# Performance work log

Hardware: AMD Instinct MI355X
Metric: run time of the kernel (lower is better)

Reference implementation:

```python
import jax, jax.numpy as jnp
import numpy as np

N_NODES = 200000
N_EDGES = 3200000
N_FEAT = 602
N_CLASS = 41


def setup_inputs() -> dict:
    key = jax.random.key(0)
    k1, k2, k3 = jax.random.split(key, 3)
    x = jax.random.normal(k1, (N_NODES, N_FEAT), dtype=jnp.float32)
    W = jax.random.normal(k2, (N_FEAT, N_CLASS), dtype=jnp.float32) * (1.0 / np.sqrt(N_FEAT))
    b = jnp.zeros((N_CLASS,), dtype=jnp.float32)
    edge_index = jax.random.randint(k3, (2, N_EDGES), 0, N_NODES, dtype=jnp.int64)
    return {"x": x, "W": W, "b": b, "edge_index": edge_index}


def reference(x, W, b, edge_index):
    # GCNConv: add self-loops, symmetric normalization, linear transform,
    # scatter-add aggregation, bias; then log_softmax (module forward).
    N = x.shape[0]
    loops = jnp.arange(N, dtype=edge_index.dtype)
    src = jnp.concatenate([edge_index[0], loops])  # [E+N]
    dst = jnp.concatenate([edge_index[1], loops])  # [E+N]
    # degree of A + I computed on destination index
    deg = jax.ops.segment_sum(jnp.ones(src.shape, dtype=x.dtype), dst, num_segments=N)
    dinv = jax.lax.rsqrt(jnp.maximum(deg, 1.0))  # deg >= 1 due to self-loops
    norm = dinv[src] * dinv[dst]                 # [E+N]
    h = x @ W                                    # [N, C] transform before aggregation (C < F)
    msg = h[src] * norm[:, None]                 # [E+N, C]
    agg = jax.ops.segment_sum(msg, dst, num_segments=N) + b  # [N, C]
    z = jax.nn.log_softmax(agg, axis=1)
    return (agg, z)
```

## Files before the change

kernel.cpp:

```cpp
#include <hip/hip_runtime.h>
#include <hip/hip_bf16.h>
#include <math.h>

#define F 602
#define C 41
#define HP_STRIDE 64
#define KSTEPS 19
#define GROWS 64
#define ASTRIDE 616

typedef short short8 __attribute__((ext_vector_type(8)));
typedef float f32x4 __attribute__((ext_vector_type(4)));

static __device__ __forceinline__ unsigned short f2bf(float f){
  unsigned int x = __float_as_uint(f);
  x += 0x7FFFu + ((x >> 16) & 1u);
  return (unsigned short)(x >> 16);
}
static __device__ __forceinline__ float bf2f(unsigned short u){
  return __uint_as_float(((unsigned int)u) << 16);
}

__global__ void k_flag(const int* __restrict__ e32, int* __restrict__ flag){
  __shared__ int s[256];
  int t = threadIdx.x;
  int v = 0;
  for (int i = t; i < 2048; i += 256) v |= e32[2*i + 1];
  s[t] = v; __syncthreads();
  for (int off = 128; off > 0; off >>= 1){
    if (t < off) s[t] |= s[t + off];
    __syncthreads();
  }
  if (t == 0) flag[0] = (s[0] == 0) ? 1 : 0;
}

static __device__ __forceinline__ int eidx(const int* __restrict__ p, int is64, long long pos){
  return is64 ? p[2*pos] : p[pos];
}

__global__ void k_count(const int* __restrict__ ei, const int* __restrict__ flag,
                        int* __restrict__ count, int* __restrict__ epos, int E){
  int e = blockIdx.x * 256 + threadIdx.x;
  if (e >= E) return;
  int is64 = flag[0];
  int d = eidx(ei, is64, (long long)E + e);
  epos[e] = atomicAdd(&count[d], 1);
}

__global__ void k_scan1(const int* __restrict__ count, int* __restrict__ rs,
                        float* __restrict__ dinv, int* __restrict__ bsum, int N){
  __shared__ int s[256];
  int t = threadIdx.x;
  int base = blockIdx.x * 2048 + t * 8;
  int v[8]; int tot = 0;
  #pragma unroll
  for (int j = 0; j < 8; j++){
    int i = base + j;
    int c = (i < N) ? count[i] : 0;
    v[j] = c; tot += c;
    if (i < N) dinv[i] = rsqrtf((float)(c + 1));
  }
  s[t] = tot; __syncthreads();
  for (int off = 1; off < 256; off <<= 1){
    int x = (t >= off) ? s[t - off] : 0;
    __syncthreads();
    s[t] += x;
    __syncthreads();
  }
  int run = s[t] - tot;
  #pragma unroll
  for (int j = 0; j < 8; j++){
    int i = base + j;
    if (i < N) rs[i] = run;
    run += v[j];
  }
  if (t == 255) bsum[blockIdx.x] = s[255];
}

__global__ void k_scan2(int* __restrict__ bsum, int nb){
  __shared__ int s[256];
  int t = threadIdx.x;
  int v = (t < nb) ? bsum[t] : 0;
  s[t] = v; __syncthreads();
  for (int off = 1; off < 256; off <<= 1){
    int x = (t >= off) ? s[t - off] : 0;
    __syncthreads();
    s[t] += x;
    __syncthreads();
  }
  if (t < nb) bsum[t] = s[t] - v;
}

__global__ void k_scan3(int* __restrict__ rs, const int* __restrict__ bsum, int N, int E){
  int i = blockIdx.x * 256 + threadIdx.x;
  if (i == 0) rs[N] = E;
  if (i >= N) return;
  rs[i] = rs[i] + bsum[i >> 11];
}

__global__ void k_fill(const int* __restrict__ ei, const int* __restrict__ flag,
                       const int* __restrict__ epos, const int* __restrict__ rs,
                       int* __restrict__ csr, int E){
  int e = blockIdx.x * 256 + threadIdx.x;
  if (e >= E) return;
  int is64 = flag[0];
  int s = eidx(ei, is64, e);
  int d = eidx(ei, is64, (long long)E + e);
  csr[rs[d] + epos[e]] = s;
}

__global__ void k_wprep(const float* __restrict__ W, unsigned short* __restrict__ Wf){
  int idx = blockIdx.x * 256 + threadIdx.x;
  if (idx >= KSTEPS * 3 * 64) return;
  int lane = idx & 63;
  int nt = (idx >> 6) % 3;
  int s = idx / (3 * 64);
  int quad = lane >> 4, l16 = lane & 15;
  int n = nt * 16 + l16;
  unsigned int w[4];
  #pragma unroll
  for (int p = 0; p < 4; p++){
    int k0 = s * 32 + quad * 8 + 2 * p;
    float lo = (k0     < F && n < C) ? W[k0 * C + n]       : 0.f;
    float hi = (k0 + 1 < F && n < C) ? W[(k0 + 1) * C + n] : 0.f;
    w[p] = (unsigned)f2bf(lo) | ((unsigned)f2bf(hi) << 16);
  }
  ((uint4*)Wf)[idx] = make_uint4(w[0], w[1], w[2], w[3]);
}

__global__ __launch_bounds__(256) void k_gemm3(const float* __restrict__ x,
        const unsigned short* __restrict__ Wf, unsigned short* __restrict__ hp, int N){
  __shared__ unsigned short As[GROWS * ASTRIDE];
  const int t = threadIdx.x;
  const long long rb0 = (long long)blockIdx.x * GROWS;
  for (int i = t; i < GROWS * 6; i += 256){
    int r = i / 6, c = 602 + (i - r * 6);
    As[r * ASTRIDE + c] = 0;
  }
  long long nrow = (long long)N - rb0; if (nrow > GROWS) nrow = GROWS;
  const int limit = (int)(nrow * F);
  const float* base = x + rb0 * F;
  #pragma unroll 8
  for (int f4 = t; f4 * 4 < limit; f4 += 256){
    int idx = f4 * 4;
    f32x4 v = __builtin_nontemporal_load((const f32x4*)(base + idx));
    int row = idx / F;
    int col = idx - row * F;
    if (col <= F - 4){
      int a = row * ASTRIDE + col;
      unsigned p0 = (unsigned)f2bf(v[0]) | ((unsigned)f2bf(v[1]) << 16);
      unsigned p1 = (unsigned)f2bf(v[2]) | ((unsigned)f2bf(v[3]) << 16);
      *(unsigned*)&As[a]     = p0;
      *(unsigned*)&As[a + 2] = p1;
    } else {
      float e[4] = {v[0], v[1], v[2], v[3]};
      #pragma unroll
      for (int q = 0; q < 4; q++){
        int ii = idx + q;
        int r2 = ii / F, c2 = ii - r2 * F;
        As[r2 * ASTRIDE + c2] = f2bf(e[q]);
      }
    }
  }
  __syncthreads();
  const int wv = t >> 6, lane = t & 63;
  const int quad = lane >> 4, l16 = lane & 15;
  const unsigned short* arow = &As[(wv * 16 + l16) * ASTRIDE + quad * 8];
  const short8* wf8 = (const short8*)Wf;
  f32x4 acc0 = {0.f,0.f,0.f,0.f}, acc1 = acc0, acc2 = acc0;
  #pragma unroll
  for (int s = 0; s < KSTEPS; s++){
    short8 a  = *(const short8*)(arow + s * 32);
    short8 b0 = wf8[(s * 3 + 0) * 64 + lane];
    short8 b1 = wf8[(s * 3 + 1) * 64 + lane];
    short8 b2 = wf8[(s * 3 + 2) * 64 + lane];
    acc0 = __builtin_amdgcn_mfma_f32_16x16x32_bf16(a, b0, acc0, 0, 0, 0);
    acc1 = __builtin_amdgcn_mfma_f32_16x16x32_bf16(a, b1, acc1, 0, 0, 0);
    acc2 = __builtin_amdgcn_mfma_f32_16x16x32_bf16(a, b2, acc2, 0, 0, 0);
  }
  int rl = wv * 16 + quad * 4;
  #pragma unroll
  for (int reg = 0; reg < 4; reg++){
    long long grow = rb0 + rl + reg;
    if (grow < N){
      unsigned short* hr = hp + grow * HP_STRIDE;
      hr[0 * 16 + l16] = f2bf(acc0[reg]);
      hr[1 * 16 + l16] = f2bf(acc1[reg]);
      hr[2 * 16 + l16] = f2bf(acc2[reg]);
    }
  }
}

__global__ __launch_bounds__(256) void k_agg(const unsigned short* __restrict__ hp,
        const int* __restrict__ csr, const int* __restrict__ rs,
        const float* __restrict__ dinv, const float* __restrict__ b,
        float* __restrict__ agg, float* __restrict__ z, int N){
  int node = blockIdx.x * 4 + (threadIdx.x >> 6);
  int lane = threadIdx.x & 63;
  if (node >= N) return;
  int beg = rs[node], end = rs[node + 1];
  float dn = dinv[node];
  bool act = lane < C;
  const unsigned short* hb = hp + lane;
  float acc = 0.f;
  if (act) acc = dn * dn * bf2f(hb[(long long)node << 6]);
  int i = beg;
  for (; i + 7 < end; i += 8){
    int s0 = csr[i],   s1 = csr[i+1], s2 = csr[i+2], s3 = csr[i+3];
    int s4 = csr[i+4], s5 = csr[i+5], s6 = csr[i+6], s7 = csr[i+7];
    float n0 = dinv[s0] * dn, n1 = dinv[s1] * dn;
    float n2 = dinv[s2] * dn, n3 = dinv[s3] * dn;
    float n4 = dinv[s4] * dn, n5 = dinv[s5] * dn;
    float n6 = dinv[s6] * dn, n7 = dinv[s7] * dn;
    float h0 = 0.f, h1 = 0.f, h2 = 0.f, h3 = 0.f;
    float h4 = 0.f, h5 = 0.f, h6 = 0.f, h7 = 0.f;
    if (act){
      h0 = bf2f(hb[(long long)s0 << 6]);
      h1 = bf2f(hb[(long long)s1 << 6]);
      h2 = bf2f(hb[(long long)s2 << 6]);
      h3 = bf2f(hb[(long long)s3 << 6]);
      h4 = bf2f(hb[(long long)s4 << 6]);
      h5 = bf2f(hb[(long long)s5 << 6]);
      h6 = bf2f(hb[(long long)s6 << 6]);
      h7 = bf2f(hb[(long long)s7 << 6]);
    }
    acc = fmaf(n0, h0, acc); acc = fmaf(n1, h1, acc);
    acc = fmaf(n2, h2, acc); acc = fmaf(n3, h3, acc);
    acc = fmaf(n4, h4, acc); acc = fmaf(n5, h5, acc);
    acc = fmaf(n6, h6, acc); acc = fmaf(n7, h7, acc);
  }
  for (; i + 3 < end; i += 4){
    int s0 = csr[i], s1 = csr[i+1], s2 = csr[i+2], s3 = csr[i+3];
    float n0 = dinv[s0] * dn, n1 = dinv[s1] * dn;
    float n2 = dinv[s2] * dn, n3 = dinv[s3] * dn;
    float h0 = 0.f, h1 = 0.f, h2 = 0.f, h3 = 0.f;
    if (act){
      h0 = bf2f(hb[(long long)s0 << 6]);
      h1 = bf2f(hb[(long long)s1 << 6]);
      h2 = bf2f(hb[(long long)s2 << 6]);
      h3 = bf2f(hb[(long long)s3 << 6]);
    }
    acc = fmaf(n0, h0, acc); acc = fmaf(n1, h1, acc);
    acc = fmaf(n2, h2, acc); acc = fmaf(n3, h3, acc);
  }
  for (; i < end; i++){
    int s0 = csr[i];
    float n0 = dinv[s0] * dn;
    if (act) acc = fmaf(n0, bf2f(hb[(long long)s0 << 6]), acc);
  }
  float a = -3.0e38f;
  if (act){
    a = acc + b[lane];
    agg[(long long)node * C + lane] = a;
  }
  float m = a;
  #pragma unroll
  for (int off = 32; off > 0; off >>= 1) m = fmaxf(m, __shfl_xor(m, off, 64));
  float ex = act ? expf(a - m) : 0.f;
  float s = ex;
  #pragma unroll
  for (int off = 32; off > 0; off >>= 1) s += __shfl_xor(s, off, 64);
  if (act) z[(long long)node * C + lane] = a - m - logf(s);
}

extern "C" void kernel_launch(void* const* d_in, const int* in_sizes, int n_in,
                              void* d_out, int out_size, void* d_ws, size_t ws_size,
                              hipStream_t stream){
  const float* x = (const float*)d_in[0];
  const float* W = (const float*)d_in[1];
  const float* b = (const float*)d_in[2];
  const int*   ei = (const int*)d_in[3];
  int N = in_sizes[0] / F;
  int E = in_sizes[3] / 2;

  float* out = (float*)d_out;
  float* agg = out;
  float* z   = out + (long long)N * C;

  char* ws = (char*)d_ws;
  auto al = [](size_t v){ return (v + 255) & ~size_t(255); };
  size_t o = 0;
  int*   flag  = (int*)(ws + o);  o = al(o + 4);
  int*   count = (int*)(ws + o);  o = al(o + (size_t)N * 4);
  float* dinv  = (float*)(ws + o); o = al(o + (size_t)N * 4);
  int*   rs    = (int*)(ws + o);  o = al(o + ((size_t)N + 1) * 4);
  int*   bsum  = (int*)(ws + o);  o = al(o + 4096);
  unsigned short* Wf = (unsigned short*)(ws + o); o = al(o + (size_t)KSTEPS * 3 * 64 * 16);
  int*   epos  = (int*)(ws + o);  o = al(o + (size_t)E * 4);
  int*   csr   = (int*)(ws + o);  o = al(o + (size_t)E * 4);
  unsigned short* hp = (unsigned short*)(ws + o); o = al(o + (size_t)N * HP_STRIDE * 2);

  int nb_e    = (E + 255) / 256;
  int nb_scan = (N + 2047) / 2048;
  int nb_n    = (N + 255) / 256;
  int nb_g    = (N + GROWS - 1) / GROWS;
  int nb_node = (N + 3) / 4;
  int nb_w    = (KSTEPS * 3 * 64 + 255) / 256;

  k_flag<<<1, 256, 0, stream>>>(ei, flag);
  hipMemsetAsync(count, 0, (size_t)N * 4, stream);
  k_count<<<nb_e, 256, 0, stream>>>(ei, flag, count, epos, E);
  k_wprep<<<nb_w, 256, 0, stream>>>(W, Wf);
  k_scan1<<<nb_scan, 256, 0, stream>>>(count, rs, dinv, bsum, N);
  k_scan2<<<1, 256, 0, stream>>>(bsum, nb_scan);
  k_scan3<<<nb_n, 256, 0, stream>>>(rs, bsum, N, E);
  k_fill<<<nb_e, 256, 0, stream>>>(ei, flag, epos, rs, csr, E);
  k_gemm3<<<nb_g, 256, 0, stream>>>(x, Wf, hp, N);
  k_agg<<<nb_node, 256, 0, stream>>>(hp, csr, rs, dinv, b, agg, z, N);
}
```

Before: 1.083 ms.

## Fuse edge counting into GEMM kernel with 8-way split counters and merged scans

Folds the atomic edge-count pass into the GEMM launch, interleaving one GEMM block with every four count blocks so atomic latency overlaps the bandwidth-bound x read. Per-destination counters are split into 8 replicas keyed by edge index to cut atomic contention, and the scan reconstructs per-replica offsets for the fill. The GEMM now reads x directly from global memory into registers instead of staging it through LDS, and scan2 is merged into scan3. In exchange it uses more workspace and memset traffic for the 8x counters, and the direct loads are narrower and less coalesced.

```diff
diff --git a/kernel.cpp b/kernel.cpp
--- a/kernel.cpp
+++ b/kernel.cpp
@@ -7,10 +7,10 @@
 #define HP_STRIDE 64
 #define KSTEPS 19
 #define GROWS 64
-#define ASTRIDE 616
 
 typedef short short8 __attribute__((ext_vector_type(8)));
 typedef float f32x4 __attribute__((ext_vector_type(4)));
+typedef float f32x2 __attribute__((ext_vector_type(2)));
 
 static __device__ __forceinline__ unsigned short f2bf(float f){
   unsigned int x = __float_as_uint(f);
@@ -36,77 +36,6 @@
 
 static __device__ __forceinline__ int eidx(const int* __restrict__ p, int is64, long long pos){
   return is64 ? p[2*pos] : p[pos];
-}
-
-__global__ void k_count(const int* __restrict__ ei, const int* __restrict__ flag,
-                        int* __restrict__ count, int* __restrict__ epos, int E){
-  int e = blockIdx.x * 256 + threadIdx.x;
-  if (e >= E) return;
-  int is64 = flag[0];
-  int d = eidx(ei, is64, (long long)E + e);
-  epos[e] = atomicAdd(&count[d], 1);
-}
-
-__global__ void k_scan1(const int* __restrict__ count, int* __restrict__ rs,
-                        float* __restrict__ dinv, int* __restrict__ bsum, int N){
-  __shared__ int s[256];
-  int t = threadIdx.x;
-  int base = blockIdx.x * 2048 + t * 8;
-  int v[8]; int tot = 0;
-  #pragma unroll
-  for (int j = 0; j < 8; j++){
-    int i = base + j;
-    int c = (i < N) ? count[i] : 0;
-    v[j] = c; tot += c;
-    if (i < N) dinv[i] = rsqrtf((float)(c + 1));
-  }
-  s[t] = tot; __syncthreads();
-  for (int off = 1; off < 256; off <<= 1){
-    int x = (t >= off) ? s[t - off] : 0;
-    __syncthreads();
-    s[t] += x;
-    __syncthreads();
-  }
-  int run = s[t] - tot;
-  #pragma unroll
-  for (int j = 0; j < 8; j++){
-    int i = base + j;
-    if (i < N) rs[i] = run;
-    run += v[j];
-  }
-  if (t == 255) bsum[blockIdx.x] = s[255];
-}
-
-__global__ void k_scan2(int* __restrict__ bsum, int nb){
-  __shared__ int s[256];
-  int t = threadIdx.x;
-  int v = (t < nb) ? bsum[t] : 0;
-  s[t] = v; __syncthreads();
-  for (int off = 1; off < 256; off <<= 1){
-    int x = (t >= off) ? s[t - off] : 0;
-    __syncthreads();
-    s[t] += x;
-    __syncthreads();
-  }
-  if (t < nb) bsum[t] = s[t] - v;
-}
-
-__global__ void k_scan3(int* __restrict__ rs, const int* __restrict__ bsum, int N, int E){
-  int i = blockIdx.x * 256 + threadIdx.x;
-  if (i == 0) rs[N] = E;
-  if (i >= N) return;
-  rs[i] = rs[i] + bsum[i >> 11];
-}
-
-__global__ void k_fill(const int* __restrict__ ei, const int* __restrict__ flag,
-                       const int* __restrict__ epos, const int* __restrict__ rs,
-                       int* __restrict__ csr, int E){
-  int e = blockIdx.x * 256 + threadIdx.x;
-  if (e >= E) return;
-  int is64 = flag[0];
-  int s = eidx(ei, is64, e);
-  int d = eidx(ei, is64, (long long)E + e);
-  csr[rs[d] + epos[e]] = s;
 }
 
 __global__ void k_wprep(const float* __restrict__ W, unsigned short* __restrict__ Wf){
@@ -128,49 +57,55 @@
   ((uint4*)Wf)[idx] = make_uint4(w[0], w[1], w[2], w[3]);
 }
 
-__global__ __launch_bounds__(256) void k_gemm3(const float* __restrict__ x,
-        const unsigned short* __restrict__ Wf, unsigned short* __restrict__ hp, int N){
-  __shared__ unsigned short As[GROWS * ASTRIDE];
+__global__ __launch_bounds__(256) void k_front(const float* __restrict__ x,
+        const unsigned short* __restrict__ Wf, unsigned short* __restrict__ hp,
+        const int* __restrict__ ei, const int* __restrict__ flag,
+        int* __restrict__ cnt8, int* __restrict__ epos,
+        int N, int E, int nb_e, int nb_g){
+  const int bid = blockIdx.x;
+  const int g = bid / 5, r5 = bid - g * 5;
+  if (r5 < 4){
+    int cb = g * 4 + r5;
+    int e = cb * 256 + threadIdx.x;
+    if (cb >= nb_e || e >= E) return;
+    int is64 = flag[0];
+    int d = eidx(ei, is64, (long long)E + e);
+    int rr = e & 7;
+    epos[e] = atomicAdd(&cnt8[(size_t)rr * N + d], 1);
+    return;
+  }
+  if (g >= nb_g) return;
   const int t = threadIdx.x;
-  const long long rb0 = (long long)blockIdx.x * GROWS;
-  for (int i = t; i < GROWS * 6; i += 256){
-    int r = i / 6, c = 602 + (i - r * 6);
-    As[r * ASTRIDE + c] = 0;
-  }
-  long long nrow = (long long)N - rb0; if (nrow > GROWS) nrow = GROWS;
-  const int limit = (int)(nrow * F);
-  const float* base = x + rb0 * F;
-  #pragma unroll 8
-  for (int f4 = t; f4 * 4 < limit; f4 += 256){
-    int idx = f4 * 4;
-    f32x4 v = __builtin_nontemporal_load((const f32x4*)(base + idx));
-    int row = idx / F;
-    int col = idx - row * F;
-    if (col <= F - 4){
-      int a = row * ASTRIDE + col;
-      unsigned p0 = (unsigned)f2bf(v[0]) | ((unsigned)f2bf(v[1]) << 16);
-      unsigned p1 = (unsigned)f2bf(v[2]) | ((unsigned)f2bf(v[3]) << 16);
-      *(unsigned*)&As[a]     = p0;
-      *(unsigned*)&As[a + 2] = p1;
-    } else {
-      float e[4] = {v[0], v[1], v[2], v[3]};
-      #pragma unroll
-      for (int q = 0; q < 4; q++){
-        int ii = idx + q;
-        int r2 = ii / F, c2 = ii - r2 * F;
-        As[r2 * ASTRIDE + c2] = f2bf(e[q]);
-      }
-    }
-  }
-  __syncthreads();
   const int wv = t >> 6, lane = t & 63;
   const int quad = lane >> 4, l16 = lane & 15;
-  const unsigned short* arow = &As[(wv * 16 + l16) * ASTRIDE + quad * 8];
+  const long long rb0 = (long long)g * GROWS;
+  long long rowb = rb0 + wv * 16 + l16;
+  long long row = (rowb < N) ? rowb : (long long)(N - 1);
+  const float* xr = x + row * (long long)F;
   const short8* wf8 = (const short8*)Wf;
+  const int kq = quad * 8;
   f32x4 acc0 = {0.f,0.f,0.f,0.f}, acc1 = acc0, acc2 = acc0;
   #pragma unroll
   for (int s = 0; s < KSTEPS; s++){
-    short8 a  = *(const short8*)(arow + s * 32);
+    float xv0, xv1, xv2, xv3, xv4, xv5, xv6, xv7;
+    if (s < KSTEPS - 1 || quad < 3){
+      int k0 = s * 32 + kq;
+      f32x2 p0 = __builtin_nontemporal_load((const f32x2*)(xr + k0 + 0));
+      f32x2 p1 = __builtin_nontemporal_load((const f32x2*)(xr + k0 + 2));
+      f32x2 p2 = __builtin_nontemporal_load((const f32x2*)(xr + k0 + 4));
+      f32x2 p3 = __builtin_nontemporal_load((const f32x2*)(xr + k0 + 6));
+      xv0 = p0[0]; xv1 = p0[1]; xv2 = p1[0]; xv3 = p1[1];
+      xv4 = p2[0]; xv5 = p2[1]; xv6 = p3[0]; xv7 = p3[1];
+    } else {
+      f32x2 p0 = __builtin_nontemporal_load((const f32x2*)(xr + 600));
+      xv0 = p0[0]; xv1 = p0[1];
+      xv2 = 0.f; xv3 = 0.f; xv4 = 0.f; xv5 = 0.f; xv6 = 0.f; xv7 = 0.f;
+    }
+    short8 a;
+    a[0] = (short)f2bf(xv0); a[1] = (short)f2bf(xv1);
+    a[2] = (short)f2bf(xv2); a[3] = (short)f2bf(xv3);
+    a[4] = (short)f2bf(xv4); a[5] = (short)f2bf(xv5);
+    a[6] = (short)f2bf(xv6); a[7] = (short)f2bf(xv7);
     short8 b0 = wf8[(s * 3 + 0) * 64 + lane];
     short8 b1 = wf8[(s * 3 + 1) * 64 + lane];
     short8 b2 = wf8[(s * 3 + 2) * 64 + lane];
@@ -189,6 +124,79 @@
       hr[2 * 16 + l16] = f2bf(acc2[reg]);
     }
   }
+}
+
+__global__ void k_scan1(const int* __restrict__ cnt8, int* __restrict__ rs,
+                        float* __restrict__ dinv, int* __restrict__ rsoff8,
+                        int* __restrict__ bsum, int N){
+  __shared__ int s[256];
+  int t = threadIdx.x;
+  int base = blockIdx.x * 2048 + t * 8;
+  int v[8]; int tot = 0;
+  #pragma unroll
+  for (int j = 0; j < 8; j++){
+    int i = base + j;
+    int c = 0;
+    if (i < N){
+      int run = 0;
+      #pragma unroll
+      for (int r = 0; r < 8; r++){
+        int cr = cnt8[(size_t)r * N + i];
+        rsoff8[(size_t)i * 8 + r] = run;
+        run += cr;
+      }
+      c = run;
+      dinv[i] = rsqrtf((float)(c + 1));
+    }
+    v[j] = c; tot += c;
+  }
+  s[t] = tot; __syncthreads();
+  for (int off = 1; off < 256; off <<= 1){
+    int x = (t >= off) ? s[t - off] : 0;
+    __syncthreads();
+    s[t] += x;
+    __syncthreads();
+  }
+  int run = s[t] - tot;
+  #pragma unroll
+  for (int j = 0; j < 8; j++){
+    int i = base + j;
+    if (i < N) rs[i] = run;
+    run += v[j];
+  }
+  if (t == 255) bsum[blockIdx.x] = s[255];
+}
+
+__global__ void k_scan3(int* __restrict__ rs, const int* __restrict__ bsum,
+                        int N, int E, int nb){
+  __shared__ int sb[256];
+  __shared__ int ex[256];
+  int t = threadIdx.x;
+  int v = (t < nb) ? bsum[t] : 0;
+  sb[t] = v; __syncthreads();
+  for (int off = 1; off < 256; off <<= 1){
+    int x = (t >= off) ? sb[t - off] : 0;
+    __syncthreads();
+    sb[t] += x;
+    __syncthreads();
+  }
+  ex[t] = sb[t] - v;
+  __syncthreads();
+  int i = blockIdx.x * 256 + t;
+  if (i == 0) rs[N] = E;
+  if (i < N) rs[i] += ex[i >> 11];
+}
+
+__global__ void k_fill(const int* __restrict__ ei, const int* __restrict__ flag,
+                       const int* __restrict__ epos, const int* __restrict__ rs,
+                       const int* __restrict__ rsoff8, int* __restrict__ csr, int E){
+  int e = blockIdx.x * 256 + threadIdx.x;
+  if (e >= E) return;
+  int is64 = flag[0];
+  int s = eidx(ei, is64, e);
+  int d = eidx(ei, is64, (long long)E + e);
+  int rr = e & 7;
+  csr[rs[d] + rsoff8[(size_t)d * 8 + rr] + epos[e]] = s;
 }
 
 __global__ __launch_bounds__(256) void k_agg(const unsigned short* __restrict__ hp,
@@ -280,31 +288,31 @@
   char* ws = (char*)d_ws;
   auto al = [](size_t v){ return (v + 255) & ~size_t(255); };
   size_t o = 0;
-  int*   flag  = (int*)(ws + o);  o = al(o + 4);
-  int*   count = (int*)(ws + o);  o = al(o + (size_t)N * 4);
-  float* dinv  = (float*)(ws + o); o = al(o + (size_t)N * 4);
-  int*   rs    = (int*)(ws + o);  o = al(o + ((size_t)N + 1) * 4);
-  int*   bsum  = (int*)(ws + o);  o = al(o + 4096);
+  int*   flag   = (int*)(ws + o);  o = al(o + 4);
+  int*   cnt8   = (int*)(ws + o);  o = al(o + (size_t)N * 8 * 4);
+  float* dinv   = (float*)(ws + o); o = al(o + (size_t)N * 4);
+  int*   rs     = (int*)(ws + o);  o = al(o + ((size_t)N + 1) * 4);
+  int*   rsoff8 = (int*)(ws + o);  o = al(o + (size_t)N * 8 * 4);
+  int*   bsum   = (int*)(ws + o);  o = al(o + 4096);
   unsigned short* Wf = (unsigned short*)(ws + o); o = al(o + (size_t)KSTEPS * 3 * 64 * 16);
-  int*   epos  = (int*)(ws + o);  o = al(o + (size_t)E * 4);
-  int*   csr   = (int*)(ws + o);  o = al(o + (size_t)E * 4);
+  int*   epos   = (int*)(ws + o);  o = al(o + (size_t)E * 4);
+  int*   csr    = (int*)(ws + o);  o = al(o + (size_t)E * 4);
   unsigned short* hp = (unsigned short*)(ws + o); o = al(o + (size_t)N * HP_STRIDE * 2);
 
   int nb_e    = (E + 255) / 256;
+  int nb_g    = (N + GROWS - 1) / GROWS;
   int nb_scan = (N + 2047) / 2048;
   int nb_n    = (N + 255) / 256;
-  int nb_g    = (N + GROWS - 1) / GROWS;
   int nb_node = (N + 3) / 4;
   int nb_w    = (KSTEPS * 3 * 64 + 255) / 256;
+  int g5      = (nb_g > (nb_e + 3) / 4) ? nb_g : (nb_e + 3) / 4;
 
   k_flag<<<1, 256, 0, stream>>>(ei, flag);
-  hipMemsetAsync(count, 0, (size_t)N * 4, stream);
-  k_count<<<nb_e, 256, 0, stream>>>(ei, flag, count, epos, E);
+  hipMemsetAsync(cnt8, 0, (size_t)N * 8 * 4, stream);
   k_wprep<<<nb_w, 256, 0, stream>>>(W, Wf);
-  k_scan1<<<nb_scan, 256, 0, stream>>>(count, rs, dinv, bsum, N);
-  k_scan2<<<1, 256, 0, stream>>>(bsum, nb_scan);
-  k_scan3<<<nb_n, 256, 0, stream>>>(rs, bsum, N, E);
-  k_fill<<<nb_e, 256, 0, stream>>>(ei, flag, epos, rs, csr, E);
-  k_gemm3<<<nb_g, 256, 0, stream>>>(x, Wf, hp, N);
+  k_front<<<5 * g5, 256, 0, stream>>>(x, Wf, hp, ei, flag, cnt8, epos, N, E, nb_e, nb_g);
+  k_scan1<<<nb_scan, 256, 0, stream>>>(cnt8, rs, dinv, rsoff8, bsum, N);
+  k_scan3<<<nb_n, 256, 0, stream>>>(rs, bsum, N, E, nb_scan);
+  k_fill<<<nb_e, 256, 0, stream>>>(ei, flag, epos, rs, rsoff8, csr, E);
   k_agg<<<nb_node, 256, 0, stream>>>(hp, csr, rs, dinv, b, agg, z, N);
 }
```

Result: no change. 1.076 ms (-0.6%).
